# Kernel optimization log

Measured on AMD Instinct MI355X. Metric: run time of the kernel, lower is better.

The kernel has to match this reference:

```python
import jax, jax.numpy as jnp
import numpy as np

B, H, F, Z, T = 8192, 256, 128, 64, 43
STEPS = T - 3


def setup_inputs() -> dict:
    key = jax.random.key(0)
    ks = jax.random.split(key, 24)
    def nrm(k, shape, s=0.05):
        return (jax.random.normal(k, shape) * s).astype(jnp.float32)
    inp = {}
    inp["h_i"] = nrm(ks[0], (B, H), 1.0)                      # encoder context state
    t = jax.random.uniform(ks[1], (B, T)) * T                  # event timestamps, sorted
    inp["input_t"] = jnp.sort(t, axis=1).astype(jnp.float32)
    inp["eps_inf"] = jax.random.normal(ks[2], (STEPS, B, Z), dtype=jnp.float32)
    inp["eps_prior"] = jax.random.normal(ks[3], (STEPS, B, Z), dtype=jnp.float32)
    in_dim = Z + H + F
    inp["Wx"] = nrm(ks[4], (in_dim, 4 * H))
    inp["Wh"] = nrm(ks[5], (H, 4 * H))
    inp["b_lstm"] = jnp.zeros((4 * H,), jnp.float32)
    dims = [(H, F), (F, F), (F, F), (2 * H + 2 * F, Z), (Z, Z), (Z, Z), (2 * H + F, Z), (Z, Z), (Z, Z)]
    for i, (di, do) in enumerate(dims, 1):
        inp[f"w{i}"] = nrm(ks[5 + i], (di, do))
        inp[f"b{i}"] = jnp.zeros((do,), jnp.float32)
    inp["alpha"] = (jax.random.uniform(ks[20], (1, 1)) * 0.1).astype(jnp.float32)
    inp["beta"] = (jax.random.uniform(ks[21], (1, 1)) * 0.1).astype(jnp.float32)
    inp["mu0"] = (jax.random.uniform(ks[22], (1, 1)) * 0.1).astype(jnp.float32)
    return inp


def _forward(h_i, input_t, eps_inf, eps_prior, Wx, Wh, b_lstm,
             w1, b1, w2, b2, w3, b3, w4, b4, w5, b5, w6, b6, w7, b7, w8, b8, w9, b9,
             alpha, beta, mu0):
    batch = h_i.shape[0]
    idxs = jnp.arange(T)

    def dense(x, w, b):
        return jax.nn.relu(x @ w + b)

    def step(carry, xs):
        h, c, z_j, y_prev = carry
        e_i, e_p, j = xs
        # LSTM cell (Keras gate order i, f, c, o)
        x = jnp.concatenate([z_j, h_i, y_prev], axis=1)
        gates = x @ Wx + h @ Wh + b_lstm
        i_g, f_g, g_g, o_g = jnp.split(gates, 4, axis=1)
        c_new = jax.nn.sigmoid(f_g) * c + jax.nn.sigmoid(i_g) * jnp.tanh(g_g)
        h_new = jax.nn.sigmoid(o_g) * jnp.tanh(c_new)
        # Hawkes intensity over events strictly before current_time_index = j+3
        t_idx = j + 3
        t_cur = jnp.take(input_t, t_idx, axis=1)[:, None]          # [B,1]
        mask = idxs < t_idx                                         # [T]
        diff = jnp.where(mask[None, :], input_t - t_cur, -jnp.inf)
        trig = jnp.sum(jnp.exp(diff), axis=1, keepdims=True) * beta[0, 0]
        intensity = mu0[0, 0] + alpha[0, 0] * trig                  # [B,1]
        # original code gates state[1] (the cell state slot) with the intensity
        c_gated = intensity * c_new
        y = dense(dense(dense(h_new, w1, b1), w2, b2), w3, b3)
        # inference network (s_j = ungated c_new, mirroring the TF code)
        inf_in = jnp.concatenate([h_i, c_new, y, y_prev], axis=1)
        hz = dense(inf_in, w4, b4)
        mean_j = dense(hz, w5, b5)
        lv_j = dense(hz, w6, b6)
        z_new = mean_j + e_i * jnp.sqrt(jnp.exp(lv_j))
        # prior network
        pri_in = jnp.concatenate([h_i, c_new, y_prev], axis=1)
        hzp = dense(pri_in, w7, b7)
        mean_p = dense(hzp, w8, b8)
        lv_p = dense(hzp, w9, b9)
        z_p = mean_p + e_p * jnp.sqrt(jnp.exp(lv_p))
        return (h_new, c_gated, z_new, y), (y, mean_j, lv_j, z_new, z_p)

    carry0 = (jnp.zeros((batch, H), h_i.dtype), jnp.zeros((batch, H), h_i.dtype),
              jnp.zeros((batch, Z), h_i.dtype), jnp.zeros((batch, F), h_i.dtype))
    xs = (eps_inf, eps_prior, jnp.arange(STEPS))
    _, (ys, means, lvs, zs, zps) = jax.lax.scan(step, carry0, xs)
    # [STEPS,B,*] -> [B,STEPS,*]
    tr = lambda a: jnp.transpose(a, (1, 0, 2))
    return tr(ys), tr(means), tr(lvs), tr(zs), tr(zps)


def reference(h_i, input_t, eps_inf, eps_prior, Wx, Wh, b_lstm,
              w1, b1, w2, b2, w3, b3, w4, b4, w5, b5, w6, b6, w7, b7, w8, b8, w9, b9,
              alpha, beta, mu0):
    return _forward(h_i, input_t, eps_inf, eps_prior, Wx, Wh, b_lstm,
                    w1, b1, w2, b2, w3, b3, w4, b4, w5, b5, w6, b6, w7, b7, w8, b8, w9, b9,
                    alpha, beta, mu0)
```

## Files before the change

### kernel.cpp

```cpp
#include <hip/hip_runtime.h>


#define BDIM  8192
#define HDIM  256
#define FDIM  128
#define ZDIM  64
#define TDIM  43
#define STEPS 40

typedef __attribute__((ext_vector_type(8))) __bf16 bf16x8;
typedef __attribute__((ext_vector_type(4))) float  f32x4;

#define ACT_STRIDE 3248
#define C_Z   0
#define C_Y0  64
#define C_Y1  192
#define C_H0  320
#define C_H1  576
#define C_C   832
#define C_T0  1088
#define C_T1  1216
#define C_HZ  1344
#define C_HZP 1408
#define C_B4  1472
#define C_B7  1536

#define PW_GS  0u
#define PW_GHI 458752u
#define PW_W1  720896u
#define PW_W2  753664u
#define PW_W3  770048u
#define PW_W4S 786432u
#define PW_W4H 819200u
#define PW_W5  835584u
#define PW_W6  839680u
#define PW_W7S 843776u
#define PW_W7H 868352u
#define PW_W8  884736u
#define PW_W9  888832u

__device__ __forceinline__ int act_off(int row, int col) {
  return row * ACT_STRIDE + ((row >> 3) << 4) + (col << 1);
}
__device__ __forceinline__ f32x4 mfma16(bf16x8 a, bf16x8 b, f32x4 c) {
  return __builtin_amdgcn_mfma_f32_16x16x32_bf16(a, b, c, 0, 0, 0);
}
__device__ __forceinline__ float sigm(float x) { return 1.f / (1.f + __expf(-x)); }
__device__ __forceinline__ float tanh_f(float x) {
  float t = __expf(-2.f * fabsf(x));
  float r = (1.f - t) / (1.f + t);
  return x < 0.f ? -r : r;
}
__device__ __forceinline__ void wg_barrier() {
  asm volatile("s_waitcnt lgkmcnt(0)" ::: "memory");
  __builtin_amdgcn_s_barrier();
  __builtin_amdgcn_sched_barrier(0);
}
__device__ __forceinline__ bf16x8 aread(const unsigned char* actb, int mt, int col,
                                        int lane) {
  return *(const bf16x8*)(actb + act_off(mt * 16 + (lane & 15), col + ((lane >> 4) << 3)));
}
__device__ __forceinline__ void st16(unsigned char* actb, int col, int mt, int rsub,
                                     f32x4 v, float bv) {
#pragma unroll
  for (int r = 0; r < 4; ++r)
    *(__bf16*)(actb + act_off(mt * 16 + rsub + r, col)) = (__bf16)fmaxf(v[r] + bv, 0.f);
}
__device__ __forceinline__ unsigned int pk2(float a, float b) {
  union { __bf16 h; unsigned short u; } x, y;
  x.h = (__bf16)a; y.h = (__bf16)b;
  return (unsigned int)x.u | ((unsigned int)y.u << 16);
}
__device__ __forceinline__ float upkf(unsigned int u, int hi) {
  union { unsigned int i; float f; } c;
  c.i = hi ? (u & 0xffff0000u) : (u << 16);
  return c.f;
}

struct PSeg { const float* p; int row0; int len; };

__global__ __launch_bounds__(256) void pack_w(PSeg s0, PSeg s1, PSeg s2,
                                              int K, int N, __bf16* __restrict__ dst) {
  int f = blockIdx.x * 256 + threadIdx.x;
  int KT = K >> 5;
  int total = KT * (N >> 4) * 64;
  if (f >= total) return;
  int lane = f & 63;
  int tile = f >> 6;
  int kt = tile % KT;
  int nt = tile / KT;
  int k0 = kt * 32 + ((lane >> 4) << 3);
  int n = (nt << 4) + (lane & 15);
  bf16x8 v;
#pragma unroll
  for (int j = 0; j < 8; ++j) {
    int k = k0 + j;
    const float* src;
    int r;
    if (k < s0.len) { src = s0.p; r = s0.row0 + k; }
    else if (k < s0.len + s1.len) { src = s1.p; r = s1.row0 + (k - s0.len); }
    else { src = s2.p; r = s2.row0 + (k - s0.len - s1.len); }
    v[j] = (__bf16)src[(size_t)r * N + n];
  }
  *(bf16x8*)(dst + (size_t)f * 8) = v;
}

struct Params {
  const float *h_i, *input_t, *eps_inf, *eps_prior;
  const float *b_lstm, *b1, *b2, *b3, *b4, *b5, *b6, *b7, *b8, *b9;
  const float *alpha, *beta, *mu0;
  const __bf16* wpack;
  float* out;
};

#define LDA(t, ktv)                                                         \
  do {                                                                      \
    _Pragma("unroll") for (int g = 0; g < 4; ++g) wb[t][g] =                \
        wgs[((size_t)(g * 16 + w) * 14 + (ktv)) * 64 + lane];               \
  } while (0)

__attribute__((amdgpu_waves_per_eu(4, 4)))
__global__ __launch_bounds__(1024) void decoder_main(Params p) {
  __shared__ __align__(16) unsigned char act[32 * ACT_STRIDE];
  __shared__ float fbuf[2048];
  __shared__ float inten[STEPS * 32];

  const int tid = threadIdx.x;
  const int w = tid >> 6;
  const int lane = tid & 63;
  const int ln16 = lane & 15;
  const int rsub = (lane >> 4) << 2;
  const int r0 = blockIdx.x * 32;

  for (int i = tid; i < (32 * ACT_STRIDE) / 4; i += 1024) ((unsigned int*)act)[i] = 0u;
  __syncthreads();
  for (int i = tid; i < 32 * 256; i += 1024) {
    int row = i >> 8, col = i & 255;
    *(__bf16*)(act + act_off(row, C_C + col)) =
        (__bf16)p.h_i[(size_t)(r0 + row) * HDIM + col];
  }
  {
    float ab = p.alpha[0] * p.beta[0], mu = p.mu0[0];
    for (int t = tid; t < 32 * STEPS; t += 1024) {
      int row = t & 31, j = t >> 5;
      const float* tp = p.input_t + (size_t)(r0 + row) * TDIM;
      float tc = tp[j + 3];
      float s = 0.f;
      for (int idx = 0; idx < j + 3; ++idx) s += __expf(tp[idx] - tc);
      inten[j * 32 + row] = mu + ab * s;
    }
  }
  __syncthreads();

  const __bf16* W = p.wpack;
  const bf16x8* wgs = (const bf16x8*)(W + PW_GS);
  const bf16x8* wghi = (const bf16x8*)(W + PW_GHI);
  const bf16x8* w1p = (const bf16x8*)(W + PW_W1);
  const bf16x8* w2p = (const bf16x8*)(W + PW_W2);
  const bf16x8* w3p = (const bf16x8*)(W + PW_W3);
  const bf16x8* w4s = (const bf16x8*)(W + PW_W4S);
  const bf16x8* w4h = (const bf16x8*)(W + PW_W4H);
  const bf16x8* w5p = (const bf16x8*)(W + PW_W5);
  const bf16x8* w6p = (const bf16x8*)(W + PW_W6);
  const bf16x8* w7s = (const bf16x8*)(W + PW_W7S);
  const bf16x8* w7h = (const bf16x8*)(W + PW_W7H);
  const bf16x8* w8p = (const bf16x8*)(W + PW_W8);
  const bf16x8* w9p = (const bf16x8*)(W + PW_W9);

  uint2 gbp[4][2];
  {
    f32x4 g[4][2] = {};
#pragma unroll
    for (int kt = 0; kt < 8; ++kt) {
      bf16x8 a0 = aread(act, 0, C_C + kt * 32, lane);
      bf16x8 a1 = aread(act, 1, C_C + kt * 32, lane);
#pragma unroll
      for (int gg = 0; gg < 4; ++gg) {
        bf16x8 b = wghi[((size_t)(gg * 16 + w) * 8 + kt) * 64 + lane];
        g[gg][0] = mfma16(a0, b, g[gg][0]);
        g[gg][1] = mfma16(a1, b, g[gg][1]);
      }
    }
#pragma unroll
    for (int gg = 0; gg < 4; ++gg) {
      float bv = p.b_lstm[gg * 256 + w * 16 + ln16];
#pragma unroll
      for (int mt = 0; mt < 2; ++mt) {
        gbp[gg][mt].x = pk2(g[gg][mt][0] + bv, g[gg][mt][1] + bv);
        gbp[gg][mt].y = pk2(g[gg][mt][2] + bv, g[gg][mt][3] + bv);
      }
    }
  }
  {
    int n = w & 3, mt = (w >> 2) & 1;
    const bf16x8* wp = (w < 8) ? w4h : w7h;
    const float* bb = (w < 8) ? p.b4 : p.b7;
    int cb = (w < 8) ? C_B4 : C_B7;
    f32x4 v = {};
#pragma unroll
    for (int kt = 0; kt < 8; ++kt)
      v = mfma16(aread(act, mt, C_C + kt * 32, lane),
                 wp[(size_t)(n * 8 + kt) * 64 + lane], v);
    float bv = bb[n * 16 + ln16];
#pragma unroll
    for (int r = 0; r < 4; ++r)
      *(__bf16*)(act + act_off(mt * 16 + rsub + r, cb + n * 16 + ln16)) =
          (__bf16)(v[r] + bv);
  }
  f32x4 c_st[2] = {};
  __syncthreads();

  float* outy = p.out;
  float* outm = p.out + (size_t)BDIM * STEPS * FDIM;
  float* outl = outm + (size_t)BDIM * STEPS * ZDIM;
  float* outz = outl + (size_t)BDIM * STEPS * ZDIM;
  float* outzp = outz + (size_t)BDIM * STEPS * ZDIM;

  bf16x8 wb[3][4];
  LDA(0, 0);
  LDA(1, 1);
  LDA(2, 2);

  for (int j = 0; j < STEPS; ++j) {
    const int yW = (j & 1) ? C_Y1 : C_Y0, yR = (j & 1) ? C_Y0 : C_Y1;
    const int hW = (j & 1) ? C_H1 : C_H0, hR = (j & 1) ? C_H0 : C_H1;

    {
      f32x4 acc[4][2] = {};
#pragma unroll
      for (int kt = 0; kt < 14; ++kt) {
        int col = (kt < 2) ? (C_Z + kt * 32)
                           : (kt < 6) ? (yR + (kt - 2) * 32) : (hR + (kt - 6) * 32);
        bf16x8 a0 = aread(act, 0, col, lane);
        bf16x8 a1 = aread(act, 1, col, lane);
        const int s = kt % 3;
#pragma unroll
        for (int g = 0; g < 4; ++g) {
          acc[g][0] = mfma16(a0, wb[s][g], acc[g][0]);
          acc[g][1] = mfma16(a1, wb[s][g], acc[g][1]);
        }
        if (kt + 3 < 14) LDA(s, kt + 3);
      }
#pragma unroll
      for (int mt = 0; mt < 2; ++mt) {
#pragma unroll
        for (int r = 0; r < 4; ++r) {
          int row = mt * 16 + rsub + r;
          unsigned int ui = (r < 2) ? gbp[0][mt].x : gbp[0][mt].y;
          unsigned int uf = (r < 2) ? gbp[1][mt].x : gbp[1][mt].y;
          unsigned int ug = (r < 2) ? gbp[2][mt].x : gbp[2][mt].y;
          unsigned int uo = (r < 2) ? gbp[3][mt].x : gbp[3][mt].y;
          float ig = sigm(acc[0][mt][r] + upkf(ui, r & 1));
          float fg = sigm(acc[1][mt][r] + upkf(uf, r & 1));
          float gg = tanh_f(acc[2][mt][r] + upkf(ug, r & 1));
          float og = sigm(acc[3][mt][r] + upkf(uo, r & 1));
          float cn = fg * c_st[mt][r] + ig * gg;
          float hn = og * tanh_f(cn);
          c_st[mt][r] = inten[j * 32 + row] * cn;
          *(__bf16*)(act + act_off(row, C_C + w * 16 + ln16)) = (__bf16)cn;
          *(__bf16*)(act + act_off(row, hW + w * 16 + ln16)) = (__bf16)hn;
        }
      }
    }
    wg_barrier();

    if (w < 8) {
      bf16x8 wf[8];
#pragma unroll
      for (int kt = 0; kt < 8; ++kt) wf[kt] = w1p[(size_t)(w * 8 + kt) * 64 + lane];
      f32x4 a0 = {}, a1 = {};
#pragma unroll
      for (int kt = 0; kt < 8; ++kt) {
        a0 = mfma16(aread(act, 0, hW + kt * 32, lane), wf[kt], a0);
        a1 = mfma16(aread(act, 1, hW + kt * 32, lane), wf[kt], a1);
      }
      float bv = p.b1[w * 16 + ln16];
      st16(act, C_T0 + w * 16 + ln16, 0, rsub, a0, bv);
      st16(act, C_T0 + w * 16 + ln16, 1, rsub, a1, bv);
    } else {
      int n = w & 3, mt = (w >> 2) & 1;
      bf16x8 wf[12];
#pragma unroll
      for (int kt = 0; kt < 12; ++kt) wf[kt] = w7s[(size_t)(n * 12 + kt) * 64 + lane];
      f32x4 v = {};
#pragma unroll
      for (int kt = 0; kt < 12; ++kt) {
        int col = (kt < 8) ? (C_C + kt * 32) : (yR + (kt - 8) * 32);
        v = mfma16(aread(act, mt, col, lane), wf[kt], v);
      }
#pragma unroll
      for (int r = 0; r < 4; ++r) {
        int row = mt * 16 + rsub + r;
        float s = v[r] + (float)*(const __bf16*)(act + act_off(row, C_B7 + n * 16 + ln16));
        *(__bf16*)(act + act_off(row, C_HZP + n * 16 + ln16)) = (__bf16)fmaxf(s, 0.f);
      }
    }
    wg_barrier();

    if (w < 8) {
      bf16x8 wf[4];
#pragma unroll
      for (int kt = 0; kt < 4; ++kt) wf[kt] = w2p[(size_t)(w * 4 + kt) * 64 + lane];
      f32x4 a0 = {}, a1 = {};
#pragma unroll
      for (int kt = 0; kt < 4; ++kt) {
        a0 = mfma16(aread(act, 0, C_T0 + kt * 32, lane), wf[kt], a0);
        a1 = mfma16(aread(act, 1, C_T0 + kt * 32, lane), wf[kt], a1);
      }
      float bv = p.b2[w * 16 + ln16];
      st16(act, C_T1 + w * 16 + ln16, 0, rsub, a0, bv);
      st16(act, C_T1 + w * 16 + ln16, 1, rsub, a1, bv);
    } else {
      int n = w & 3, mt = (w >> 2) & 1;
      float ep[4];
#pragma unroll
      for (int r = 0; r < 4; ++r)
        ep[r] = __builtin_nontemporal_load(
            p.eps_prior + ((size_t)j * BDIM + r0 + mt * 16 + rsub + r) * ZDIM +
            n * 16 + ln16);
      bf16x8 wm[2], wl[2];
#pragma unroll
      for (int kt = 0; kt < 2; ++kt) {
        wm[kt] = w8p[(size_t)(n * 2 + kt) * 64 + lane];
        wl[kt] = w9p[(size_t)(n * 2 + kt) * 64 + lane];
      }
      f32x4 vm = {}, vl = {};
#pragma unroll
      for (int kt = 0; kt < 2; ++kt) {
        bf16x8 a = aread(act, mt, C_HZP + kt * 32, lane);
        vm = mfma16(a, wm[kt], vm);
        vl = mfma16(a, wl[kt], vl);
      }
      float bm = p.b8[n * 16 + ln16], bl = p.b9[n * 16 + ln16];
#pragma unroll
      for (int r = 0; r < 4; ++r) {
        int row = mt * 16 + rsub + r, col = n * 16 + ln16;
        float mp = fmaxf(vm[r] + bm, 0.f), lp = fmaxf(vl[r] + bl, 0.f);
        float zp = mp + ep[r] * __expf(0.5f * lp);
        __builtin_nontemporal_store(
            zp, outzp + ((size_t)(r0 + row) * STEPS + j) * ZDIM + col);
      }
    }
    wg_barrier();

    if (w < 8) {
      bf16x8 wf[4];
#pragma unroll
      for (int kt = 0; kt < 4; ++kt) wf[kt] = w3p[(size_t)(w * 4 + kt) * 64 + lane];
      f32x4 a0 = {}, a1 = {};
#pragma unroll
      for (int kt = 0; kt < 4; ++kt) {
        a0 = mfma16(aread(act, 0, C_T1 + kt * 32, lane), wf[kt], a0);
        a1 = mfma16(aread(act, 1, C_T1 + kt * 32, lane), wf[kt], a1);
      }
      float bv = p.b3[w * 16 + ln16];
#pragma unroll
      for (int mt = 0; mt < 2; ++mt) {
        f32x4 vv = mt ? a1 : a0;
#pragma unroll
        for (int r = 0; r < 4; ++r) {
          int row = mt * 16 + rsub + r;
          float yv = fmaxf(vv[r] + bv, 0.f);
          *(__bf16*)(act + act_off(row, yW + w * 16 + ln16)) = (__bf16)yv;
          __builtin_nontemporal_store(
              yv, outy + ((size_t)(r0 + row) * STEPS + j) * FDIM + w * 16 + ln16);
        }
      }
    } else {
      int a = w - 8, n = a & 3, mt = a >> 2;
      bf16x8 wf[12];
#pragma unroll
      for (int kk = 0; kk < 12; ++kk) {
        int kt = (kk < 8) ? kk : (kk + 4);
        wf[kk] = w4s[(size_t)(n * 16 + kt) * 64 + lane];
      }
      f32x4 v = {};
#pragma unroll
      for (int kk = 0; kk < 12; ++kk) {
        int col = (kk < 8) ? (C_C + kk * 32) : (yR + (kk - 8) * 32);
        v = mfma16(aread(act, mt, col, lane), wf[kk], v);
      }
#pragma unroll
      for (int r = 0; r < 4; ++r)
        fbuf[(mt * 16 + rsub + r) * 64 + n * 16 + ln16] = v[r];
    }
    wg_barrier();

    LDA(0, 0);
    LDA(1, 1);
    LDA(2, 2);
    if (w < 8) {
      int n = w & 3, mt = w >> 2;
      bf16x8 wf[4];
#pragma unroll
      for (int kt = 8; kt < 12; ++kt) wf[kt - 8] = w4s[(size_t)(n * 16 + kt) * 64 + lane];
      f32x4 v = {};
#pragma unroll
      for (int kt = 8; kt < 12; ++kt)
        v = mfma16(aread(act, mt, yW + (kt - 8) * 32, lane), wf[kt - 8], v);
#pragma unroll
      for (int r = 0; r < 4; ++r) {
        int row = mt * 16 + rsub + r, cc = n * 16 + ln16;
        float s = v[r] + fbuf[row * 64 + cc] +
                  (float)*(const __bf16*)(act + act_off(row, C_B4 + cc));
        *(__bf16*)(act + act_off(row, C_HZ + cc)) = (__bf16)fmaxf(s, 0.f);
      }
    }
    wg_barrier();

    if (w < 8) {
      int n = w & 3, mt = w >> 2;
      float ei[4];
#pragma unroll
      for (int r = 0; r < 4; ++r)
        ei[r] = __builtin_nontemporal_load(
            p.eps_inf + ((size_t)j * BDIM + r0 + mt * 16 + rsub + r) * ZDIM +
            n * 16 + ln16);
      bf16x8 wm[2], wl[2];
#pragma unroll
      for (int kt = 0; kt < 2; ++kt) {
        wm[kt] = w5p[(size_t)(n * 2 + kt) * 64 + lane];
        wl[kt] = w6p[(size_t)(n * 2 + kt) * 64 + lane];
      }
      f32x4 vm = {}, vl = {};
#pragma unroll
      for (int kt = 0; kt < 2; ++kt) {
        bf16x8 a = aread(act, mt, C_HZ + kt * 32, lane);
        vm = mfma16(a, wm[kt], vm);
        vl = mfma16(a, wl[kt], vl);
      }
      float bm = p.b5[n * 16 + ln16], bl = p.b6[n * 16 + ln16];
#pragma unroll
      for (int r = 0; r < 4; ++r) {
        int row = mt * 16 + rsub + r, col = n * 16 + ln16;
        float m = fmaxf(vm[r] + bm, 0.f), l = fmaxf(vl[r] + bl, 0.f);
        float zn = m + ei[r] * __expf(0.5f * l);
        size_t ob = ((size_t)(r0 + row) * STEPS + j) * ZDIM + col;
        __builtin_nontemporal_store(m, outm + ob);
        __builtin_nontemporal_store(l, outl + ob);
        __builtin_nontemporal_store(zn, outz + ob);
        *(__bf16*)(act + act_off(row, C_Z + col)) = (__bf16)zn;
      }
    }
    wg_barrier();
  }
}

extern "C" void kernel_launch(void* const* d_in, const int* in_sizes, int n_in,
                              void* d_out, int out_size, void* d_ws, size_t ws_size,
                              hipStream_t stream) {
  const float* h_i = (const float*)d_in[0];
  const float* input_t = (const float*)d_in[1];
  const float* eps_inf = (const float*)d_in[2];
  const float* eps_prior = (const float*)d_in[3];
  const float* Wx = (const float*)d_in[4];
  const float* Wh = (const float*)d_in[5];
  const float* b_lstm = (const float*)d_in[6];
  const float* w1 = (const float*)d_in[7];  const float* b1 = (const float*)d_in[8];
  const float* w2 = (const float*)d_in[9];  const float* b2 = (const float*)d_in[10];
  const float* w3 = (const float*)d_in[11]; const float* b3 = (const float*)d_in[12];
  const float* w4 = (const float*)d_in[13]; const float* b4 = (const float*)d_in[14];
  const float* w5 = (const float*)d_in[15]; const float* b5 = (const float*)d_in[16];
  const float* w6 = (const float*)d_in[17]; const float* b6 = (const float*)d_in[18];
  const float* w7 = (const float*)d_in[19]; const float* b7 = (const float*)d_in[20];
  const float* w8 = (const float*)d_in[21]; const float* b8 = (const float*)d_in[22];
  const float* w9 = (const float*)d_in[23]; const float* b9 = (const float*)d_in[24];
  const float* alpha = (const float*)d_in[25];
  const float* beta = (const float*)d_in[26];
  const float* mu0 = (const float*)d_in[27];
  __bf16* ws = (__bf16*)d_ws;

  auto S = [](const float* ptr, int row0, int len) {
    PSeg s; s.p = ptr; s.row0 = row0; s.len = len; return s;
  };
  PSeg Zs; Zs.p = nullptr; Zs.row0 = 0; Zs.len = 0;
  auto L = [&](PSeg a, PSeg b, PSeg c, int K, int N, unsigned off) {
    int total = (K / 32) * (N / 16) * 64;
    pack_w<<<(total + 255) / 256, 256, 0, stream>>>(a, b, c, K, N, ws + off);
  };
  L(S(Wx, 0, 64), S(Wx, 320, 128), S(Wh, 0, 256), 448, 1024, PW_GS);
  L(S(Wx, 64, 256), Zs, Zs, 256, 1024, PW_GHI);
  L(S(w1, 0, 256), Zs, Zs, 256, 128, PW_W1);
  L(S(w2, 0, 128), Zs, Zs, 128, 128, PW_W2);
  L(S(w3, 0, 128), Zs, Zs, 128, 128, PW_W3);
  L(S(w4, 256, 512), Zs, Zs, 512, 64, PW_W4S);
  L(S(w4, 0, 256), Zs, Zs, 256, 64, PW_W4H);
  L(S(w5, 0, 64), Zs, Zs, 64, 64, PW_W5);
  L(S(w6, 0, 64), Zs, Zs, 64, 64, PW_W6);
  L(S(w7, 256, 384), Zs, Zs, 384, 64, PW_W7S);
  L(S(w7, 0, 256), Zs, Zs, 256, 64, PW_W7H);
  L(S(w8, 0, 64), Zs, Zs, 64, 64, PW_W8);
  L(S(w9, 0, 64), Zs, Zs, 64, 64, PW_W9);

  Params p;
  p.h_i = h_i; p.input_t = input_t; p.eps_inf = eps_inf; p.eps_prior = eps_prior;
  p.b_lstm = b_lstm; p.b1 = b1; p.b2 = b2; p.b3 = b3; p.b4 = b4; p.b5 = b5;
  p.b6 = b6; p.b7 = b7; p.b8 = b8; p.b9 = b9;
  p.alpha = alpha; p.beta = beta; p.mu0 = mu0;
  p.wpack = ws;
  p.out = (float*)d_out;

  decoder_main<<<256, 1024, 0, stream>>>(p);
}
```

Measured before the change: 2.403 ms.

## Halve rows per block to 16 with 8 waves and software-pipelined gate weight loads

Each workgroup now handles 16 batch rows with 512 threads (8 waves), so the launch uses 512 blocks instead of 256, and the work split across waves is rebuilt around one M-tile. The LSTM gate GEMM streams weights through two register buffers using inline-asm global loads with explicit vmcnt waits, so weight fetches overlap the MFMA work. The h_i-dependent w4/w7 contributions and biases are kept in registers instead of LDS. The fbuf split of the w4 reduction is removed, and the stage layout is rebalanced between the prior and inference branches. The trade-off is that each weight byte is reused across half as many rows, so more weight traffic goes through L2.

Measured after the change: 4.538 ms. 1.89x slower.

```diff
diff --git a/kernel.cpp b/kernel.cpp
--- a/kernel.cpp
+++ b/kernel.cpp
@@ -7,9 +7,11 @@
 #define ZDIM  64
 #define TDIM  43
 #define STEPS 40
+#define ROWS  16
 
 typedef __attribute__((ext_vector_type(8))) __bf16 bf16x8;
 typedef __attribute__((ext_vector_type(4))) float  f32x4;
+typedef __attribute__((ext_vector_type(4))) int    i32x4;
 
 #define ACT_STRIDE 3248
 #define C_Z   0
@@ -22,8 +24,6 @@
 #define C_T1  1216
 #define C_HZ  1344
 #define C_HZP 1408
-#define C_B4  1472
-#define C_B7  1536
 
 #define PW_GS  0u
 #define PW_GHI 458752u
@@ -39,6 +39,13 @@
 #define PW_W8  884736u
 #define PW_W9  888832u
 
+#define SB() __builtin_amdgcn_sched_barrier(0)
+#define VMW(N)                                             \
+  do {                                                     \
+    asm volatile("s_waitcnt vmcnt(" #N ")" ::: "memory");  \
+    SB();                                                  \
+  } while (0)
+
 __device__ __forceinline__ int act_off(int row, int col) {
   return row * ACT_STRIDE + ((row >> 3) << 4) + (col << 1);
 }
@@ -56,15 +63,19 @@
   __builtin_amdgcn_s_barrier();
   __builtin_amdgcn_sched_barrier(0);
 }
-__device__ __forceinline__ bf16x8 aread(const unsigned char* actb, int mt, int col,
-                                        int lane) {
-  return *(const bf16x8*)(actb + act_off(mt * 16 + (lane & 15), col + ((lane >> 4) << 3)));
-}
-__device__ __forceinline__ void st16(unsigned char* actb, int col, int mt, int rsub,
-                                     f32x4 v, float bv) {
+__device__ __forceinline__ bf16x8 gld(const bf16x8* p) {
+  i32x4 r;
+  asm volatile("global_load_dwordx4 %0, %1, off" : "=v"(r) : "v"(p));
+  return __builtin_bit_cast(bf16x8, r);
+}
+__device__ __forceinline__ bf16x8 aread(const unsigned char* a, int col, int lane) {
+  return *(const bf16x8*)(a + act_off(lane & 15, col + ((lane >> 4) << 3)));
+}
+__device__ __forceinline__ void st16(unsigned char* a, int col, int rsub, f32x4 v,
+                                     float bv) {
 #pragma unroll
   for (int r = 0; r < 4; ++r)
-    *(__bf16*)(actb + act_off(mt * 16 + rsub + r, col)) = (__bf16)fmaxf(v[r] + bv, 0.f);
+    *(__bf16*)(a + act_off(rsub + r, col)) = (__bf16)fmaxf(v[r] + bv, 0.f);
 }
 __device__ __forceinline__ unsigned int pk2(float a, float b) {
   union { __bf16 h; unsigned short u; } x, y;
@@ -113,41 +124,44 @@
   float* out;
 };
 
-#define LDA(t, ktv)                                                         \
-  do {                                                                      \
-    _Pragma("unroll") for (int g = 0; g < 4; ++g) wb[t][g] =                \
-        wgs[((size_t)(g * 16 + w) * 14 + (ktv)) * 64 + lane];               \
-  } while (0)
-
-__attribute__((amdgpu_waves_per_eu(4, 4)))
-__global__ __launch_bounds__(1024) void decoder_main(Params p) {
-  __shared__ __align__(16) unsigned char act[32 * ACT_STRIDE];
-  __shared__ float fbuf[2048];
-  __shared__ float inten[STEPS * 32];
+__device__ __forceinline__ void issueG(bf16x8 (&wf)[4], const bf16x8* wgs, int w,
+                                       int lane, int kt, int g2) {
+#pragma unroll
+  for (int i = 0; i < 4; ++i) {
+    int g = g2 * 2 + (i >> 1), hh = i & 1;
+    wf[i] = gld(wgs + ((size_t)((g * 16 + hh * 8 + w) * 14 + kt) << 6) + lane);
+  }
+}
+
+__global__ __launch_bounds__(512) __attribute__((amdgpu_waves_per_eu(4, 4)))
+void decoder_main(Params p) {
+  __shared__ __align__(16) unsigned char act[ROWS * ACT_STRIDE + 16];
+  __shared__ float inten[STEPS * ROWS];
 
   const int tid = threadIdx.x;
   const int w = tid >> 6;
   const int lane = tid & 63;
   const int ln16 = lane & 15;
   const int rsub = (lane >> 4) << 2;
-  const int r0 = blockIdx.x * 32;
-
-  for (int i = tid; i < (32 * ACT_STRIDE) / 4; i += 1024) ((unsigned int*)act)[i] = 0u;
+  const int r0 = blockIdx.x * ROWS;
+
+  for (int i = tid; i < (ROWS * ACT_STRIDE + 16) / 4; i += 512)
+    ((unsigned int*)act)[i] = 0u;
   __syncthreads();
-  for (int i = tid; i < 32 * 256; i += 1024) {
+  for (int i = tid; i < ROWS * 256; i += 512) {
     int row = i >> 8, col = i & 255;
     *(__bf16*)(act + act_off(row, C_C + col)) =
         (__bf16)p.h_i[(size_t)(r0 + row) * HDIM + col];
   }
   {
     float ab = p.alpha[0] * p.beta[0], mu = p.mu0[0];
-    for (int t = tid; t < 32 * STEPS; t += 1024) {
-      int row = t & 31, j = t >> 5;
+    for (int t = tid; t < ROWS * STEPS; t += 512) {
+      int row = t & (ROWS - 1), j = t >> 4;
       const float* tp = p.input_t + (size_t)(r0 + row) * TDIM;
       float tc = tp[j + 3];
       float s = 0.f;
       for (int idx = 0; idx < j + 3; ++idx) s += __expf(tp[idx] - tc);
-      inten[j * 32 + row] = mu + ab * s;
+      inten[j * ROWS + row] = mu + ab * s;
     }
   }
   __syncthreads();
@@ -169,43 +183,64 @@
 
   uint2 gbp[4][2];
   {
-    f32x4 g[4][2] = {};
+    f32x4 g4[4][2] = {};
 #pragma unroll
     for (int kt = 0; kt < 8; ++kt) {
-      bf16x8 a0 = aread(act, 0, C_C + kt * 32, lane);
-      bf16x8 a1 = aread(act, 1, C_C + kt * 32, lane);
-#pragma unroll
-      for (int gg = 0; gg < 4; ++gg) {
-        bf16x8 b = wghi[((size_t)(gg * 16 + w) * 8 + kt) * 64 + lane];
-        g[gg][0] = mfma16(a0, b, g[gg][0]);
-        g[gg][1] = mfma16(a1, b, g[gg][1]);
-      }
-    }
-#pragma unroll
-    for (int gg = 0; gg < 4; ++gg) {
-      float bv = p.b_lstm[gg * 256 + w * 16 + ln16];
-#pragma unroll
-      for (int mt = 0; mt < 2; ++mt) {
-        gbp[gg][mt].x = pk2(g[gg][mt][0] + bv, g[gg][mt][1] + bv);
-        gbp[gg][mt].y = pk2(g[gg][mt][2] + bv, g[gg][mt][3] + bv);
-      }
-    }
-  }
+      bf16x8 a = aread(act, C_C + kt * 32, lane);
+#pragma unroll
+      for (int g = 0; g < 4; ++g)
+#pragma unroll
+        for (int hh = 0; hh < 2; ++hh) {
+          bf16x8 b = wghi[((size_t)((g * 16 + hh * 8 + w) * 8 + kt)) * 64 + lane];
+          g4[g][hh] = mfma16(a, b, g4[g][hh]);
+        }
+    }
+#pragma unroll
+    for (int g = 0; g < 4; ++g)
+#pragma unroll
+      for (int hh = 0; hh < 2; ++hh) {
+        float bv = p.b_lstm[g * 256 + hh * 128 + w * 16 + ln16];
+        gbp[g][hh].x = pk2(g4[g][hh][0] + bv, g4[g][hh][1] + bv);
+        gbp[g][hh].y = pk2(g4[g][hh][2] + bv, g4[g][hh][3] + bv);
+      }
+  }
+  const int nr = (w < 4) ? w : (w - 4);
+  f32x4 foldv = {};
+  bf16x8 wA[2], wB[2];
+  float bA, bB;
   {
-    int n = w & 3, mt = (w >> 2) & 1;
-    const bf16x8* wp = (w < 8) ? w4h : w7h;
-    const float* bb = (w < 8) ? p.b4 : p.b7;
-    int cb = (w < 8) ? C_B4 : C_B7;
+    const bf16x8* wph = (w < 4) ? w4h : w7h;
+    const float* bbh = (w < 4) ? p.b4 : p.b7;
     f32x4 v = {};
 #pragma unroll
     for (int kt = 0; kt < 8; ++kt)
-      v = mfma16(aread(act, mt, C_C + kt * 32, lane),
-                 wp[(size_t)(n * 8 + kt) * 64 + lane], v);
-    float bv = bb[n * 16 + ln16];
-#pragma unroll
-    for (int r = 0; r < 4; ++r)
-      *(__bf16*)(act + act_off(mt * 16 + rsub + r, cb + n * 16 + ln16)) =
-          (__bf16)(v[r] + bv);
+      v = mfma16(aread(act, C_C + kt * 32, lane),
+                 wph[(size_t)(nr * 8 + kt) * 64 + lane], v);
+    float bv = bbh[nr * 16 + ln16];
+#pragma unroll
+    for (int r = 0; r < 4; ++r) foldv[r] = v[r] + bv;
+    const bf16x8* wpa = (w < 4) ? w5p : w8p;
+    const bf16x8* wpb = (w < 4) ? w6p : w9p;
+#pragma unroll
+    for (int kt = 0; kt < 2; ++kt) {
+      wA[kt] = wpa[(size_t)(nr * 2 + kt) * 64 + lane];
+      wB[kt] = wpb[(size_t)(nr * 2 + kt) * 64 + lane];
+    }
+    bA = ((w < 4) ? p.b5 : p.b8)[nr * 16 + ln16];
+    bB = ((w < 4) ? p.b6 : p.b9)[nr * 16 + ln16];
+  }
+  const float bi = p.b_lstm[0];
+  (void)bi;
+  const float bv1 = p.b1[w * 16 + ln16];
+  float bv2 = 0.f, bv3 = 0.f;
+  if (w < 4) {
+    bv2 = p.b2[w * 16 + ln16];
+    bv3 = p.b3[w * 16 + ln16];
+  }
+  float bv2b = 0.f, bv3b = 0.f;
+  if (w < 4) {
+    bv2b = p.b2[(4 + w) * 16 + ln16];
+    bv3b = p.b3[(4 + w) * 16 + ln16];
   }
   f32x4 c_st[2] = {};
   __syncthreads();
@@ -216,224 +251,204 @@
   float* outz = outl + (size_t)BDIM * STEPS * ZDIM;
   float* outzp = outz + (size_t)BDIM * STEPS * ZDIM;
 
-  bf16x8 wb[3][4];
-  LDA(0, 0);
-  LDA(1, 1);
-  LDA(2, 2);
+  bf16x8 X[4], Y[4];
+  issueG(X, wgs, w, lane, 0, 0);
+  issueG(Y, wgs, w, lane, 0, 1);
 
   for (int j = 0; j < STEPS; ++j) {
     const int yW = (j & 1) ? C_Y1 : C_Y0, yR = (j & 1) ? C_Y0 : C_Y1;
     const int hW = (j & 1) ? C_H1 : C_H0, hR = (j & 1) ? C_H0 : C_H1;
 
     {
-      f32x4 acc[4][2] = {};
+      f32x4 acc[4][2];
+#pragma unroll
+      for (int g = 0; g < 4; ++g)
+#pragma unroll
+        for (int hh = 0; hh < 2; ++hh) {
+          acc[g][hh][0] = upkf(gbp[g][hh].x, 0);
+          acc[g][hh][1] = upkf(gbp[g][hh].x, 1);
+          acc[g][hh][2] = upkf(gbp[g][hh].y, 0);
+          acc[g][hh][3] = upkf(gbp[g][hh].y, 1);
+        }
 #pragma unroll
       for (int kt = 0; kt < 14; ++kt) {
         int col = (kt < 2) ? (C_Z + kt * 32)
                            : (kt < 6) ? (yR + (kt - 2) * 32) : (hR + (kt - 6) * 32);
-        bf16x8 a0 = aread(act, 0, col, lane);
-        bf16x8 a1 = aread(act, 1, col, lane);
-        const int s = kt % 3;
-#pragma unroll
-        for (int g = 0; g < 4; ++g) {
-          acc[g][0] = mfma16(a0, wb[s][g], acc[g][0]);
-          acc[g][1] = mfma16(a1, wb[s][g], acc[g][1]);
-        }
-        if (kt + 3 < 14) LDA(s, kt + 3);
-      }
-#pragma unroll
-      for (int mt = 0; mt < 2; ++mt) {
+        bf16x8 a = aread(act, col, lane);
+        VMW(4);
+#pragma unroll
+        for (int i = 0; i < 4; ++i)
+          acc[(i >> 1)][i & 1] = mfma16(a, X[i], acc[(i >> 1)][i & 1]);
+        SB();
+        if (kt + 1 < 14) issueG(X, wgs, w, lane, kt + 1, 0);
+        if (kt + 1 < 14) { VMW(4); } else { VMW(0); }
+#pragma unroll
+        for (int i = 0; i < 4; ++i)
+          acc[2 + (i >> 1)][i & 1] = mfma16(a, Y[i], acc[2 + (i >> 1)][i & 1]);
+        SB();
+        if (kt + 1 < 14) issueG(Y, wgs, w, lane, kt + 1, 1);
+      }
+#pragma unroll
+      for (int hh = 0; hh < 2; ++hh) {
+        int colc = hh * 128 + w * 16 + ln16;
 #pragma unroll
         for (int r = 0; r < 4; ++r) {
-          int row = mt * 16 + rsub + r;
-          unsigned int ui = (r < 2) ? gbp[0][mt].x : gbp[0][mt].y;
-          unsigned int uf = (r < 2) ? gbp[1][mt].x : gbp[1][mt].y;
-          unsigned int ug = (r < 2) ? gbp[2][mt].x : gbp[2][mt].y;
-          unsigned int uo = (r < 2) ? gbp[3][mt].x : gbp[3][mt].y;
-          float ig = sigm(acc[0][mt][r] + upkf(ui, r & 1));
-          float fg = sigm(acc[1][mt][r] + upkf(uf, r & 1));
-          float gg = tanh_f(acc[2][mt][r] + upkf(ug, r & 1));
-          float og = sigm(acc[3][mt][r] + upkf(uo, r & 1));
-          float cn = fg * c_st[mt][r] + ig * gg;
+          int row = rsub + r;
+          float ig = sigm(acc[0][hh][r]);
+          float fg = sigm(acc[1][hh][r]);
+          float gg = tanh_f(acc[2][hh][r]);
+          float og = sigm(acc[3][hh][r]);
+          float cn = fg * c_st[hh][r] + ig * gg;
           float hn = og * tanh_f(cn);
-          c_st[mt][r] = inten[j * 32 + row] * cn;
-          *(__bf16*)(act + act_off(row, C_C + w * 16 + ln16)) = (__bf16)cn;
-          *(__bf16*)(act + act_off(row, hW + w * 16 + ln16)) = (__bf16)hn;
+          c_st[hh][r] = inten[j * ROWS + row] * cn;
+          *(__bf16*)(act + act_off(row, C_C + colc)) = (__bf16)cn;
+          *(__bf16*)(act + act_off(row, hW + colc)) = (__bf16)hn;
         }
       }
     }
     wg_barrier();
 
-    if (w < 8) {
+    {
       bf16x8 wf[8];
 #pragma unroll
-      for (int kt = 0; kt < 8; ++kt) wf[kt] = w1p[(size_t)(w * 8 + kt) * 64 + lane];
-      f32x4 a0 = {}, a1 = {};
-#pragma unroll
-      for (int kt = 0; kt < 8; ++kt) {
-        a0 = mfma16(aread(act, 0, hW + kt * 32, lane), wf[kt], a0);
-        a1 = mfma16(aread(act, 1, hW + kt * 32, lane), wf[kt], a1);
-      }
-      float bv = p.b1[w * 16 + ln16];
-      st16(act, C_T0 + w * 16 + ln16, 0, rsub, a0, bv);
-      st16(act, C_T0 + w * 16 + ln16, 1, rsub, a1, bv);
-    } else {
-      int n = w & 3, mt = (w >> 2) & 1;
-      bf16x8 wf[12];
-#pragma unroll
-      for (int kt = 0; kt < 12; ++kt) wf[kt] = w7s[(size_t)(n * 12 + kt) * 64 + lane];
+      for (int kt = 0; kt < 8; ++kt)
+        wf[kt] = gld(w1p + (size_t)(w * 8 + kt) * 64 + lane);
+      VMW(0);
       f32x4 v = {};
 #pragma unroll
-      for (int kt = 0; kt < 12; ++kt) {
-        int col = (kt < 8) ? (C_C + kt * 32) : (yR + (kt - 8) * 32);
-        v = mfma16(aread(act, mt, col, lane), wf[kt], v);
+      for (int kt = 0; kt < 8; ++kt)
+        v = mfma16(aread(act, hW + kt * 32, lane), wf[kt], v);
+      st16(act, C_T0 + w * 16 + ln16, rsub, v, bv1);
+    }
+    wg_barrier();
+
+    {
+      if (w < 4) {
+        bf16x8 wf[8];
+#pragma unroll
+        for (int kt = 0; kt < 4; ++kt) {
+          wf[kt] = gld(w2p + (size_t)(w * 4 + kt) * 64 + lane);
+          wf[4 + kt] = gld(w2p + (size_t)((4 + w) * 4 + kt) * 64 + lane);
+        }
+        VMW(0);
+        f32x4 v0 = {}, v1 = {};
+#pragma unroll
+        for (int kt = 0; kt < 4; ++kt) {
+          bf16x8 a = aread(act, C_T0 + kt * 32, lane);
+          v0 = mfma16(a, wf[kt], v0);
+          v1 = mfma16(a, wf[4 + kt], v1);
+        }
+        st16(act, C_T1 + w * 16 + ln16, rsub, v0, bv2);
+        st16(act, C_T1 + (4 + w) * 16 + ln16, rsub, v1, bv2b);
+      } else {
+        bf16x8 wf[12];
+#pragma unroll
+        for (int kt = 0; kt < 12; ++kt)
+          wf[kt] = gld(w7s + (size_t)(nr * 12 + kt) * 64 + lane);
+        VMW(0);
+        f32x4 v = {};
+#pragma unroll
+        for (int kt = 0; kt < 12; ++kt) {
+          int col = (kt < 8) ? (C_C + kt * 32) : (yR + (kt - 8) * 32);
+          v = mfma16(aread(act, col, lane), wf[kt], v);
+        }
+#pragma unroll
+        for (int r = 0; r < 4; ++r)
+          *(__bf16*)(act + act_off(rsub + r, C_HZP + nr * 16 + ln16)) =
+              (__bf16)fmaxf(v[r] + foldv[r], 0.f);
+      }
+    }
+    wg_barrier();
+
+    {
+      if (w < 4) {
+        bf16x8 wf[8];
+#pragma unroll
+        for (int kt = 0; kt < 4; ++kt) {
+          wf[kt] = gld(w3p + (size_t)(w * 4 + kt) * 64 + lane);
+          wf[4 + kt] = gld(w3p + (size_t)((4 + w) * 4 + kt) * 64 + lane);
+        }
+        VMW(0);
+        f32x4 v0 = {}, v1 = {};
+#pragma unroll
+        for (int kt = 0; kt < 4; ++kt) {
+          bf16x8 a = aread(act, C_T1 + kt * 32, lane);
+          v0 = mfma16(a, wf[kt], v0);
+          v1 = mfma16(a, wf[4 + kt], v1);
+        }
+#pragma unroll
+        for (int r = 0; r < 4; ++r) {
+          int row = rsub + r;
+          float y0 = fmaxf(v0[r] + bv3, 0.f);
+          float y1 = fmaxf(v1[r] + bv3b, 0.f);
+          *(__bf16*)(act + act_off(row, yW + w * 16 + ln16)) = (__bf16)y0;
+          *(__bf16*)(act + act_off(row, yW + 64 + w * 16 + ln16)) = (__bf16)y1;
+          size_t ob = ((size_t)(r0 + row) * STEPS + j) * FDIM;
+          __builtin_nontemporal_store(y0, outy + ob + w * 16 + ln16);
+          __builtin_nontemporal_store(y1, outy + ob + 64 + w * 16 + ln16);
+        }
+      } else {
+        float ep[4];
+#pragma unroll
+        for (int r = 0; r < 4; ++r)
+          ep[r] = p.eps_prior[((size_t)j * BDIM + r0 + rsub + r) * ZDIM +
+                              nr * 16 + ln16];
+        f32x4 vm = {}, vl = {};
+#pragma unroll
+        for (int kt = 0; kt < 2; ++kt) {
+          bf16x8 a = aread(act, C_HZP + kt * 32, lane);
+          vm = mfma16(a, wA[kt], vm);
+          vl = mfma16(a, wB[kt], vl);
+        }
+#pragma unroll
+        for (int r = 0; r < 4; ++r) {
+          float mp = fmaxf(vm[r] + bA, 0.f), lp = fmaxf(vl[r] + bB, 0.f);
+          float zp = mp + ep[r] * __expf(0.5f * lp);
+          __builtin_nontemporal_store(
+              zp, outzp + ((size_t)(r0 + rsub + r) * STEPS + j) * ZDIM +
+                      nr * 16 + ln16);
+        }
+      }
+    }
+    wg_barrier();
+
+    float ei[4];
+    if (w < 4) {
+      bf16x8 wf[16];
+#pragma unroll
+      for (int kt = 0; kt < 16; ++kt)
+        wf[kt] = gld(w4s + (size_t)(nr * 16 + kt) * 64 + lane);
+#pragma unroll
+      for (int r = 0; r < 4; ++r)
+        ei[r] = p.eps_inf[((size_t)j * BDIM + r0 + rsub + r) * ZDIM +
+                          nr * 16 + ln16];
+      VMW(0);
+      f32x4 v = {};
+#pragma unroll
+      for (int kt = 0; kt < 16; ++kt) {
+        int col = (kt < 8) ? (C_C + kt * 32)
+                           : (kt < 12) ? (yW + (kt - 8) * 32) : (yR + (kt - 12) * 32);
+        v = mfma16(aread(act, col, lane), wf[kt], v);
+      }
+#pragma unroll
+      for (int r = 0; r < 4; ++r)
+        *(__bf16*)(act + act_off(rsub + r, C_HZ + nr * 16 + ln16)) =
+            (__bf16)fmaxf(v[r] + foldv[r], 0.f);
+    }
+    wg_barrier();
+
+    if (w < 4) {
+      f32x4 vm = {}, vl = {};
+#pragma unroll
+      for (int kt = 0; kt < 2; ++kt) {
+        bf16x8 a = aread(act, C_HZ + kt * 32, lane);
+        vm = mfma16(a, wA[kt], vm);
+        vl = mfma16(a, wB[kt], vl);
       }
 #pragma unroll
       for (int r = 0; r < 4; ++r) {
-        int row = mt * 16 + rsub + r;
-        float s = v[r] + (float)*(const __bf16*)(act + act_off(row, C_B7 + n * 16 + ln16));
-        *(__bf16*)(act + act_off(row, C_HZP + n * 16 + ln16)) = (__bf16)fmaxf(s, 0.f);
-      }
-    }
-    wg_barrier();
-
-    if (w < 8) {
-      bf16x8 wf[4];
-#pragma unroll
-      for (int kt = 0; kt < 4; ++kt) wf[kt] = w2p[(size_t)(w * 4 + kt) * 64 + lane];
-      f32x4 a0 = {}, a1 = {};
-#pragma unroll
-      for (int kt = 0; kt < 4; ++kt) {
-        a0 = mfma16(aread(act, 0, C_T0 + kt * 32, lane), wf[kt], a0);
-        a1 = mfma16(aread(act, 1, C_T0 + kt * 32, lane), wf[kt], a1);
-      }
-      float bv = p.b2[w * 16 + ln16];
-      st16(act, C_T1 + w * 16 + ln16, 0, rsub, a0, bv);
-      st16(act, C_T1 + w * 16 + ln16, 1, rsub, a1, bv);
-    } else {
-      int n = w & 3, mt = (w >> 2) & 1;
-      float ep[4];
-#pragma unroll
-      for (int r = 0; r < 4; ++r)
-        ep[r] = __builtin_nontemporal_load(
-            p.eps_prior + ((size_t)j * BDIM + r0 + mt * 16 + rsub + r) * ZDIM +
-            n * 16 + ln16);
-      bf16x8 wm[2], wl[2];
-#pragma unroll
-      for (int kt = 0; kt < 2; ++kt) {
-        wm[kt] = w8p[(size_t)(n * 2 + kt) * 64 + lane];
-        wl[kt] = w9p[(size_t)(n * 2 + kt) * 64 + lane];
-      }
-      f32x4 vm = {}, vl = {};
-#pragma unroll
-      for (int kt = 0; kt < 2; ++kt) {
-        bf16x8 a = aread(act, mt, C_HZP + kt * 32, lane);
-        vm = mfma16(a, wm[kt], vm);
-        vl = mfma16(a, wl[kt], vl);
-      }
-      float bm = p.b8[n * 16 + ln16], bl = p.b9[n * 16 + ln16];
-#pragma unroll
-      for (int r = 0; r < 4; ++r) {
-        int row = mt * 16 + rsub + r, col = n * 16 + ln16;
-        float mp = fmaxf(vm[r] + bm, 0.f), lp = fmaxf(vl[r] + bl, 0.f);
-        float zp = mp + ep[r] * __expf(0.5f * lp);
-        __builtin_nontemporal_store(
-            zp, outzp + ((size_t)(r0 + row) * STEPS + j) * ZDIM + col);
-      }
-    }
-    wg_barrier();
-
-    if (w < 8) {
-      bf16x8 wf[4];
-#pragma unroll
-      for (int kt = 0; kt < 4; ++kt) wf[kt] = w3p[(size_t)(w * 4 + kt) * 64 + lane];
-      f32x4 a0 = {}, a1 = {};
-#pragma unroll
-      for (int kt = 0; kt < 4; ++kt) {
-        a0 = mfma16(aread(act, 0, C_T1 + kt * 32, lane), wf[kt], a0);
-        a1 = mfma16(aread(act, 1, C_T1 + kt * 32, lane), wf[kt], a1);
-      }
-      float bv = p.b3[w * 16 + ln16];
-#pragma unroll
-      for (int mt = 0; mt < 2; ++mt) {
-        f32x4 vv = mt ? a1 : a0;
-#pragma unroll
-        for (int r = 0; r < 4; ++r) {
-          int row = mt * 16 + rsub + r;
-          float yv = fmaxf(vv[r] + bv, 0.f);
-          *(__bf16*)(act + act_off(row, yW + w * 16 + ln16)) = (__bf16)yv;
-          __builtin_nontemporal_store(
-              yv, outy + ((size_t)(r0 + row) * STEPS + j) * FDIM + w * 16 + ln16);
-        }
-      }
-    } else {
-      int a = w - 8, n = a & 3, mt = a >> 2;
-      bf16x8 wf[12];
-#pragma unroll
-      for (int kk = 0; kk < 12; ++kk) {
-        int kt = (kk < 8) ? kk : (kk + 4);
-        wf[kk] = w4s[(size_t)(n * 16 + kt) * 64 + lane];
-      }
-      f32x4 v = {};
-#pragma unroll
-      for (int kk = 0; kk < 12; ++kk) {
-        int col = (kk < 8) ? (C_C + kk * 32) : (yR + (kk - 8) * 32);
-        v = mfma16(aread(act, mt, col, lane), wf[kk], v);
-      }
-#pragma unroll
-      for (int r = 0; r < 4; ++r)
-        fbuf[(mt * 16 + rsub + r) * 64 + n * 16 + ln16] = v[r];
-    }
-    wg_barrier();
-
-    LDA(0, 0);
-    LDA(1, 1);
-    LDA(2, 2);
-    if (w < 8) {
-      int n = w & 3, mt = w >> 2;
-      bf16x8 wf[4];
-#pragma unroll
-      for (int kt = 8; kt < 12; ++kt) wf[kt - 8] = w4s[(size_t)(n * 16 + kt) * 64 + lane];
-      f32x4 v = {};
-#pragma unroll
-      for (int kt = 8; kt < 12; ++kt)
-        v = mfma16(aread(act, mt, yW + (kt - 8) * 32, lane), wf[kt - 8], v);
-#pragma unroll
-      for (int r = 0; r < 4; ++r) {
-        int row = mt * 16 + rsub + r, cc = n * 16 + ln16;
-        float s = v[r] + fbuf[row * 64 + cc] +
-                  (float)*(const __bf16*)(act + act_off(row, C_B4 + cc));
-        *(__bf16*)(act + act_off(row, C_HZ + cc)) = (__bf16)fmaxf(s, 0.f);
-      }
-    }
-    wg_barrier();
-
-    if (w < 8) {
-      int n = w & 3, mt = w >> 2;
-      float ei[4];
-#pragma unroll
-      for (int r = 0; r < 4; ++r)
-        ei[r] = __builtin_nontemporal_load(
-            p.eps_inf + ((size_t)j * BDIM + r0 + mt * 16 + rsub + r) * ZDIM +
-            n * 16 + ln16);
-      bf16x8 wm[2], wl[2];
-#pragma unroll
-      for (int kt = 0; kt < 2; ++kt) {
-        wm[kt] = w5p[(size_t)(n * 2 + kt) * 64 + lane];
-        wl[kt] = w6p[(size_t)(n * 2 + kt) * 64 + lane];
-      }
-      f32x4 vm = {}, vl = {};
-#pragma unroll
-      for (int kt = 0; kt < 2; ++kt) {
-        bf16x8 a = aread(act, mt, C_HZ + kt * 32, lane);
-        vm = mfma16(a, wm[kt], vm);
-        vl = mfma16(a, wl[kt], vl);
-      }
-      float bm = p.b5[n * 16 + ln16], bl = p.b6[n * 16 + ln16];
-#pragma unroll
-      for (int r = 0; r < 4; ++r) {
-        int row = mt * 16 + rsub + r, col = n * 16 + ln16;
-        float m = fmaxf(vm[r] + bm, 0.f), l = fmaxf(vl[r] + bl, 0.f);
+        int row = rsub + r, col = nr * 16 + ln16;
+        float m = fmaxf(vm[r] + bA, 0.f), l = fmaxf(vl[r] + bB, 0.f);
         float zn = m + ei[r] * __expf(0.5f * l);
         size_t ob = ((size_t)(r0 + row) * STEPS + j) * ZDIM + col;
         __builtin_nontemporal_store(m, outm + ob);
@@ -442,6 +457,8 @@
         *(__bf16*)(act + act_off(row, C_Z + col)) = (__bf16)zn;
       }
     }
+    issueG(X, wgs, w, lane, 0, 0);
+    issueG(Y, wgs, w, lane, 0, 1);
     wg_barrier();
   }
 }
@@ -500,5 +517,5 @@
   p.wpack = ws;
   p.out = (float*)d_out;
 
-  decoder_main<<<256, 1024, 0, stream>>>(p);
-}
+  decoder_main<<<512, 512, 0, stream>>>(p);
+}
```
